# Performance work log

Measured on AMD Instinct MI355X. Metric: run time of the kernel, lower is better.

Reference implementation:

```python
import jax, jax.numpy as jnp
from jax import lax
import numpy as np

B = 128          # batch size
S = 207          # input spatial size implied by outputSpatialSize=[8,8]
N_PTS = 256000
NEG = -1e30      # -inf stand-in for masked max-pooling
# BNReLU channel counts in execution order: 8 resnet blocks x (bn1, bn2), final resnet BN(32), last BN(64)
SIZES = [8,8,8,8,8,16,16,16,16,24,24,24,24,32,32,32,32,64]
OFF = np.cumsum([0] + SIZES)

WSHAPES = dict(conv0=(3,3,1,8),
               c1a=(3,3,8,8), c1b=(3,3,8,8), c2a=(3,3,8,8), c2b=(3,3,8,8),
               c3a=(3,3,8,16), c3b=(3,3,16,16), c3r=(3,3,8,16),
               c4a=(3,3,16,16), c4b=(3,3,16,16),
               c5a=(3,3,16,24), c5b=(3,3,24,24), c5r=(3,3,16,24),
               c6a=(3,3,24,24), c6b=(3,3,24,24),
               c7a=(3,3,24,32), c7b=(3,3,32,32), c7r=(3,3,24,32),
               c8a=(3,3,32,32), c8b=(3,3,32,32),
               conv_last=(5,5,32,64))

def _conv(x, w, stride, padding):
    return lax.conv_general_dilated(x, w, (stride, stride), padding,
                                    dimension_numbers=('NHWC', 'HWIO', 'NHWC'))

def _pool_max(x, win, stride, init):
    return lax.reduce_window(x, init, lax.max, (1, win, win, 1), (1, stride, stride, 1), 'VALID')

def _bnrelu(x, m, g, b):
    # eval-mode BN folded to affine, applied on active sites only (inactive stay exactly 0)
    return m * jax.nn.relu(x * g + b)

def _subconv(x, w, m):
    # submanifold conv == dense conv on zero-filled grid, output restricted to active sites
    return _conv(x, w, 1, 'SAME') * m

def _strided(x, w, m, win, stride):
    # scn.Convolution: output site active iff any active input in its receptive field
    m2 = _pool_max(m, win, stride, 0.0)
    return _conv(x, w, stride, 'VALID') * m2, m2

def _block(x, m, g1, b1, w1, g2, b2, w2, wres, stride):
    # pre-activation basic block from scn.SparseResNet
    h = _bnrelu(x, m, g1, b1)
    if stride == 1:
        h, m2 = _subconv(h, w1, m), m
    else:
        h, m2 = _strided(h, w1, m, 3, 2)
    h = _subconv(_bnrelu(h, m2, g2, b2), w2, m2)
    r = x if wres is None else _strided(x, wres, m, 3, 2)[0]
    return h + r, m2

def _forward(locations, batch_idx, features, bn_gamma, bn_beta, W):
    idx = (batch_idx, locations[:, 0], locations[:, 1], jnp.zeros_like(batch_idx))
    x = jnp.zeros((B, S, S, 1), jnp.float32).at[idx].add(features[:, 0])  # InputLayer (sum dups)
    m = jnp.zeros((B, S, S, 1), jnp.float32).at[idx].set(1.0)             # active-site mask
    g = [bn_gamma[OFF[i]:OFF[i+1]] for i in range(len(SIZES))]
    b = [bn_beta[OFF[i]:OFF[i+1]] for i in range(len(SIZES))]
    x = _subconv(x, W['conv0'], m)                              # 1->8 @ 207x207
    # MaxPooling(pool 3, stride 2) over active sites only
    m2 = _pool_max(m, 3, 2, 0.0)
    x = jnp.where(m2 > 0, _pool_max(jnp.where(m > 0, x, NEG), 3, 2, NEG), 0.0)
    m = m2                                                      # @ 103x103
    blocks = [('c1a', 'c1b', None, 1), ('c2a', 'c2b', None, 1),
              ('c3a', 'c3b', 'c3r', 2), ('c4a', 'c4b', None, 1),
              ('c5a', 'c5b', 'c5r', 2), ('c6a', 'c6b', None, 1),
              ('c7a', 'c7b', 'c7r', 2), ('c8a', 'c8b', None, 1)]
    for i, (k1, k2, kr, st) in enumerate(blocks):
        x, m = _block(x, m, g[2*i], b[2*i], W[k1], g[2*i+1], b[2*i+1], W[k2],
                      None if kr is None else W[kr], st)        # 103->51->25->12
    x = _bnrelu(x, m, g[16], b[16])                             # final resnet BNReLU(32)
    x, m = _strided(x, W['conv_last'], m, 5, 1)                 # 32->64, 12x12 -> 8x8
    x = _bnrelu(x, m, g[17], b[17])
    flat = x.transpose(0, 3, 1, 2).reshape(B, -1)               # SparseToDense + flatten (NCHW order)
    return (flat @ W['w_lin'].T).reshape(B, -1, 1)              # [B, 100, 1]

def setup_inputs():
    key = jax.random.key(0)
    ks = iter(jax.random.split(key, 64))
    inp = {
        'locations': jax.random.randint(next(ks), (N_PTS, 2), 0, S, dtype=jnp.int32),
        'batch_idx': jax.random.randint(next(ks), (N_PTS,), 0, B, dtype=jnp.int32),
        'features': jax.random.normal(next(ks), (N_PTS, 1), jnp.float32),
        'bn_gamma': 1.0 + 0.1 * jax.random.normal(next(ks), (int(OFF[-1]),), jnp.float32),
        'bn_beta': 0.1 * jax.random.normal(next(ks), (int(OFF[-1]),), jnp.float32),
    }
    for name, shp in WSHAPES.items():
        fan_in = int(np.prod(shp[:-1]))
        inp[name] = jax.random.normal(next(ks), shp, jnp.float32) * (2.0 / fan_in) ** 0.5
    inp['w_lin'] = jax.random.normal(next(ks), (100, 64 * 8 * 8), jnp.float32) * (1.0 / 4096.0) ** 0.5
    return inp

def reference(locations, batch_idx, features, bn_gamma, bn_beta, conv0,
              c1a, c1b, c2a, c2b, c3a, c3b, c3r, c4a, c4b, c5a, c5b, c5r,
              c6a, c6b, c7a, c7b, c7r, c8a, c8b, conv_last, w_lin):
    W = dict(conv0=conv0, c1a=c1a, c1b=c1b, c2a=c2a, c2b=c2b, c3a=c3a, c3b=c3b, c3r=c3r,
             c4a=c4a, c4b=c4b, c5a=c5a, c5b=c5b, c5r=c5r, c6a=c6a, c6b=c6b,
             c7a=c7a, c7b=c7b, c7r=c7r, c8a=c8a, c8b=c8b, conv_last=conv_last, w_lin=w_lin)
    return _forward(locations, batch_idx, features, bn_gamma, bn_beta, W)
```

## Files before the change

kernel.cpp:

```cpp
#include <hip/hip_runtime.h>

#define S 207
#define BATCH 128
#define NPTS 256000

static const int OFFS[19] = {0,8,16,24,32,40,56,72,88,104,128,152,176,200,232,264,296,328,392};

__global__ void zero2_kernel(float4* __restrict__ a, float4* __restrict__ b, int n4) {
    int i = blockIdx.x * blockDim.x + threadIdx.x;
    if (i < n4) { a[i] = make_float4(0,0,0,0); b[i] = make_float4(0,0,0,0); }
}

__global__ void zero_kernel(float* __restrict__ p, int n) {
    int i = blockIdx.x * blockDim.x + threadIdx.x;
    if (i < n) p[i] = 0.0f;
}

__global__ void scatter_kernel(const int* __restrict__ loc, const int* __restrict__ bidx,
                               const float* __restrict__ feat,
                               float* __restrict__ xs, float* __restrict__ ms) {
    int t = blockIdx.x * blockDim.x + threadIdx.x;
    if (t >= NPTS) return;
    int b = bidx[t];
    int r = loc[2 * t];
    int c = loc[2 * t + 1];
    int idx = (b * S + r) * S + c;
    atomicAdd(&xs[idx], feat[t]);
    ms[idx] = 1.0f;
}

__global__ __launch_bounds__(256) void conv0_pool_kernel(
    const float* __restrict__ xs, const float* __restrict__ ms,
    const float* __restrict__ w,
    float* __restrict__ x1, float* __restrict__ m1) {
    const int Hout = 103;
    int opix = blockIdx.x * 256 + threadIdx.x;
    int total = BATCH * Hout * Hout;
    if (opix >= total) return;
    int wo = opix % Hout;
    int t = opix / Hout;
    int ho = t % Hout;
    int b  = t / Hout;

    float mv[3][3];
    float mwin = 0.0f;
    #pragma unroll
    for (int pi = 0; pi < 3; ++pi)
        #pragma unroll
        for (int pj = 0; pj < 3; ++pj) {
            float m = ms[(b * S + 2 * ho + pi) * S + 2 * wo + pj];
            mv[pi][pj] = m;
            mwin = fmaxf(mwin, m);
        }
    float* xp = x1 + (size_t)opix * 8;
    if (mwin <= 0.0f) {
        *(float4*)xp = make_float4(0,0,0,0);
        *(float4*)(xp + 4) = make_float4(0,0,0,0);
        m1[opix] = 0.0f;
        return;
    }
    float p[5][5];
    #pragma unroll
    for (int r = 0; r < 5; ++r) {
        int ii = 2 * ho - 1 + r;
        #pragma unroll
        for (int c = 0; c < 5; ++c) {
            int jj = 2 * wo - 1 + c;
            bool ok = ((unsigned)ii < (unsigned)S) && ((unsigned)jj < (unsigned)S);
            p[r][c] = ok ? xs[(b * S + ii) * S + jj] : 0.0f;
        }
    }
    float best[8];
    #pragma unroll
    for (int co = 0; co < 8; ++co) best[co] = -1e30f;
    #pragma unroll
    for (int pi = 0; pi < 3; ++pi)
        #pragma unroll
        for (int pj = 0; pj < 3; ++pj) {
            if (mv[pi][pj] > 0.0f) {
                float acc[8];
                #pragma unroll
                for (int co = 0; co < 8; ++co) acc[co] = 0.0f;
                #pragma unroll
                for (int kh = 0; kh < 3; ++kh)
                    #pragma unroll
                    for (int kw = 0; kw < 3; ++kw) {
                        float x = p[pi + kh][pj + kw];
                        #pragma unroll
                        for (int co = 0; co < 8; ++co)
                            acc[co] = fmaf(x, w[(kh * 3 + kw) * 8 + co], acc[co]);
                    }
                #pragma unroll
                for (int co = 0; co < 8; ++co) best[co] = fmaxf(best[co], acc[co]);
            }
        }
    *(float4*)xp = make_float4(best[0], best[1], best[2], best[3]);
    *(float4*)(xp + 4) = make_float4(best[4], best[5], best[6], best[7]);
    m1[opix] = 1.0f;
}

template <int C, int TILE, int NTX>
__global__ __launch_bounds__(256) void resblock_kernel(
    const float* __restrict__ in, const float* __restrict__ mask,
    const float* __restrict__ w1, const float* __restrict__ w2,
    const float* __restrict__ g1, const float* __restrict__ bb1,
    const float* __restrict__ g2, const float* __restrict__ bb2,
    float* __restrict__ out, int H) {
    constexpr int XT = TILE + 4, HT = TILE + 2;
    constexpr int XA = XT * XT, HA = HT * HT;
    __shared__ float xs[C][XA];
    __shared__ float h1[C][HA];
    __shared__ float msh[XA];

    int tid = threadIdx.x;
    int bid = blockIdx.x;
    int b = bid / (NTX * NTX);
    int t = bid % (NTX * NTX);
    int r0 = (t / NTX) * TILE, c0 = (t % NTX) * TILE;

    float gr[C], br[C];
    #pragma unroll
    for (int c = 0; c < C; ++c) { gr[c] = g1[c]; br[c] = bb1[c]; }

    for (int i = tid; i < XA; i += 256) {
        int py = i / XT, px = i % XT;
        int gy = r0 - 2 + py, gx = c0 - 2 + px;
        bool ok = (unsigned)gy < (unsigned)H && (unsigned)gx < (unsigned)H;
        float m = 0.0f;
        if (ok) m = mask[(size_t)(b * H + gy) * H + gx];
        msh[i] = m;
        if (m > 0.0f) {
            const float* ip = in + ((size_t)(b * H + gy) * H + gx) * C;
            #pragma unroll
            for (int c = 0; c < C; c += 4) {
                float4 x4 = *(const float4*)(ip + c);
                xs[c    ][i] = m * fmaxf(fmaf(x4.x, gr[c],     br[c]),     0.0f);
                xs[c + 1][i] = m * fmaxf(fmaf(x4.y, gr[c + 1], br[c + 1]), 0.0f);
                xs[c + 2][i] = m * fmaxf(fmaf(x4.z, gr[c + 2], br[c + 2]), 0.0f);
                xs[c + 3][i] = m * fmaxf(fmaf(x4.w, gr[c + 3], br[c + 3]), 0.0f);
            }
        } else {
            #pragma unroll
            for (int c = 0; c < C; ++c) xs[c][i] = 0.0f;
        }
    }
    #pragma unroll
    for (int c = 0; c < C; ++c) { gr[c] = g2[c]; br[c] = bb2[c]; }
    __syncthreads();

    for (int pos = tid; pos < HA; pos += 256) {
        int py = pos / HT, px = pos % HT;
        float mc = msh[(py + 1) * XT + px + 1];
        float acc[C];
        #pragma unroll
        for (int co = 0; co < C; ++co) acc[co] = 0.0f;
        if (mc > 0.0f) {
            #pragma unroll
            for (int kh = 0; kh < 3; ++kh)
                #pragma unroll
                for (int kw = 0; kw < 3; ++kw) {
                    int pix = (py + kh) * XT + px + kw;
                    const float* wp = w1 + (kh * 3 + kw) * C * C;
                    #pragma unroll
                    for (int ci = 0; ci < C; ++ci) {
                        float xv = xs[ci][pix];
                        #pragma unroll
                        for (int co = 0; co < C; ++co)
                            acc[co] = fmaf(xv, wp[ci * C + co], acc[co]);
                    }
                }
        }
        #pragma unroll
        for (int co = 0; co < C; ++co)
            h1[co][pos] = mc * fmaxf(fmaf(acc[co] * mc, gr[co], br[co]), 0.0f);
    }
    __syncthreads();

    for (int pos = tid; pos < TILE * TILE; pos += 256) {
        int ty = pos / TILE, tx = pos % TILE;
        int gy = r0 + ty, gx = c0 + tx;
        if (gy < H && gx < H) {
            float mo = msh[(ty + 2) * XT + tx + 2];
            float acc[C];
            #pragma unroll
            for (int co = 0; co < C; ++co) acc[co] = 0.0f;
            if (mo > 0.0f) {
                #pragma unroll
                for (int kh = 0; kh < 3; ++kh)
                    #pragma unroll
                    for (int kw = 0; kw < 3; ++kw) {
                        int pix = (ty + kh) * HT + tx + kw;
                        const float* wp = w2 + (kh * 3 + kw) * C * C;
                        #pragma unroll
                        for (int ci = 0; ci < C; ++ci) {
                            float xv = h1[ci][pix];
                            #pragma unroll
                            for (int co = 0; co < C; ++co)
                                acc[co] = fmaf(xv, wp[ci * C + co], acc[co]);
                        }
                    }
            }
            const float* rp = in + ((size_t)(b * H + gy) * H + gx) * C;
            float* op = out + ((size_t)(b * H + gy) * H + gx) * C;
            #pragma unroll
            for (int j = 0; j < C; j += 4) {
                float4 r4 = *(const float4*)(rp + j);
                float4 o4;
                o4.x = fmaf(acc[j],     mo, r4.x);
                o4.y = fmaf(acc[j + 1], mo, r4.y);
                o4.z = fmaf(acc[j + 2], mo, r4.z);
                o4.w = fmaf(acc[j + 3], mo, r4.w);
                *(float4*)(op + j) = o4;
            }
        }
    }
}

template <int K, int CIN, int COUT, int COT, bool BN, bool RES>
__global__ __launch_bounds__(256) void fconv_kernel(
    const float* __restrict__ in, const float* __restrict__ w,
    const float* __restrict__ g, const float* __restrict__ bbn,
    const float* __restrict__ mIn, const float* __restrict__ mOut,
    const float* __restrict__ res, float* __restrict__ out,
    int Hin, int Hout, int stride, int pad) {
    const int Win = Hin, Wout = Hout;
    int npix = BATCH * Hout * Wout;
    int opix = blockIdx.x * 256 + threadIdx.x;
    if (opix >= npix) return;
    int co0 = blockIdx.y * COT;
    int wo = opix % Wout;
    int t = opix / Wout;
    int ho = t % Hout;
    int b  = t / Hout;

    float mo = mOut[opix];
    float* op = out + (size_t)opix * COUT + co0;
    if (mo <= 0.0f) {
        #pragma unroll
        for (int j = 0; j < COT; j += 4) {
            float4 r4 = RES ? *(const float4*)(res + (size_t)opix * COUT + co0 + j)
                            : make_float4(0,0,0,0);
            *(float4*)(op + j) = r4;
        }
        return;
    }
    float acc[COT];
    #pragma unroll
    for (int j = 0; j < COT; ++j) acc[j] = 0.0f;

    #pragma unroll
    for (int kh = 0; kh < K; ++kh) {
        int ih = ho * stride + kh - pad;
        if ((unsigned)ih >= (unsigned)Hin) continue;
        #pragma unroll
        for (int kw = 0; kw < K; ++kw) {
            int iw = wo * stride + kw - pad;
            if ((unsigned)iw >= (unsigned)Win) continue;
            int ipix = (b * Hin + ih) * Win + iw;
            float mi = 1.0f;
            if (BN) { mi = mIn[ipix]; if (mi <= 0.0f) continue; }
            const float* ip = in + (size_t)ipix * CIN;
            const float* wp = w + (kh * K + kw) * CIN * COUT + co0;
            #pragma unroll
            for (int ci = 0; ci < CIN; ci += 4) {
                float4 xv = *(const float4*)(ip + ci);
                if (BN) {
                    xv.x = mi * fmaxf(fmaf(xv.x, g[ci],     bbn[ci]),     0.0f);
                    xv.y = mi * fmaxf(fmaf(xv.y, g[ci + 1], bbn[ci + 1]), 0.0f);
                    xv.z = mi * fmaxf(fmaf(xv.z, g[ci + 2], bbn[ci + 2]), 0.0f);
                    xv.w = mi * fmaxf(fmaf(xv.w, g[ci + 3], bbn[ci + 3]), 0.0f);
                }
                #pragma unroll
                for (int j = 0; j < COT; ++j) {
                    acc[j] = fmaf(xv.x, wp[(ci    ) * COUT + j], acc[j]);
                    acc[j] = fmaf(xv.y, wp[(ci + 1) * COUT + j], acc[j]);
                    acc[j] = fmaf(xv.z, wp[(ci + 2) * COUT + j], acc[j]);
                    acc[j] = fmaf(xv.w, wp[(ci + 3) * COUT + j], acc[j]);
                }
            }
        }
    }
    #pragma unroll
    for (int j = 0; j < COT; j += 4) {
        float4 o4;
        o4.x = acc[j] * mo; o4.y = acc[j+1] * mo; o4.z = acc[j+2] * mo; o4.w = acc[j+3] * mo;
        if (RES) {
            float4 r4 = *(const float4*)(res + (size_t)opix * COUT + co0 + j);
            o4.x += r4.x; o4.y += r4.y; o4.z += r4.z; o4.w += r4.w;
        }
        *(float4*)(op + j) = o4;
    }
}

template <int CIN, int COUT, int COT>
__global__ __launch_bounds__(256) void strided_both_kernel(
    const float* __restrict__ in,
    const float* __restrict__ wR, const float* __restrict__ wA,
    const float* __restrict__ g, const float* __restrict__ bbn,
    const float* __restrict__ mIn, float* __restrict__ mOutBuf,
    float* __restrict__ outR, float* __restrict__ outA,
    int Hin, int Hout) {
    int npix = BATCH * Hout * Hout;
    int opix = blockIdx.x * 256 + threadIdx.x;
    if (opix >= npix) return;
    int co0 = blockIdx.y * COT;
    int wo = opix % Hout;
    int t = opix / Hout;
    int ho = t % Hout;
    int b  = t / Hout;

    float accR[COT], accA[COT];
    #pragma unroll
    for (int j = 0; j < COT; ++j) { accR[j] = 0.0f; accA[j] = 0.0f; }
    float m2 = 0.0f;

    #pragma unroll
    for (int kh = 0; kh < 3; ++kh) {
        int ih = 2 * ho + kh;
        #pragma unroll
        for (int kw = 0; kw < 3; ++kw) {
            int iw = 2 * wo + kw;
            int ipix = (b * Hin + ih) * Hin + iw;
            float mi = mIn[ipix];
            if (mi <= 0.0f) continue;
            m2 = fmaxf(m2, mi);
            const float* ip  = in + (size_t)ipix * CIN;
            const float* wpR = wR + (kh * 3 + kw) * CIN * COUT + co0;
            const float* wpA = wA + (kh * 3 + kw) * CIN * COUT + co0;
            #pragma unroll
            for (int ci = 0; ci < CIN; ci += 4) {
                float4 xv = *(const float4*)(ip + ci);
                float4 xa;
                xa.x = mi * fmaxf(fmaf(xv.x, g[ci],     bbn[ci]),     0.0f);
                xa.y = mi * fmaxf(fmaf(xv.y, g[ci + 1], bbn[ci + 1]), 0.0f);
                xa.z = mi * fmaxf(fmaf(xv.z, g[ci + 2], bbn[ci + 2]), 0.0f);
                xa.w = mi * fmaxf(fmaf(xv.w, g[ci + 3], bbn[ci + 3]), 0.0f);
                #pragma unroll
                for (int j = 0; j < COT; ++j) {
                    accR[j] = fmaf(xv.x, wpR[(ci    ) * COUT + j], accR[j]);
                    accR[j] = fmaf(xv.y, wpR[(ci + 1) * COUT + j], accR[j]);
                    accR[j] = fmaf(xv.z, wpR[(ci + 2) * COUT + j], accR[j]);
                    accR[j] = fmaf(xv.w, wpR[(ci + 3) * COUT + j], accR[j]);
                    accA[j] = fmaf(xa.x, wpA[(ci    ) * COUT + j], accA[j]);
                    accA[j] = fmaf(xa.y, wpA[(ci + 1) * COUT + j], accA[j]);
                    accA[j] = fmaf(xa.z, wpA[(ci + 2) * COUT + j], accA[j]);
                    accA[j] = fmaf(xa.w, wpA[(ci + 3) * COUT + j], accA[j]);
                }
            }
        }
    }
    if (blockIdx.y == 0) mOutBuf[opix] = m2;
    float* opR = outR + (size_t)opix * COUT + co0;
    float* opA = outA + (size_t)opix * COUT + co0;
    #pragma unroll
    for (int j = 0; j < COT; j += 4) {
        *(float4*)(opR + j) = make_float4(accR[j] * m2, accR[j+1] * m2, accR[j+2] * m2, accR[j+3] * m2);
        *(float4*)(opA + j) = make_float4(accA[j] * m2, accA[j+1] * m2, accA[j+2] * m2, accA[j+3] * m2);
    }
}

__global__ __launch_bounds__(256) void convlast_kernel(
    const float* __restrict__ in,
    const float* __restrict__ w,
    const float* __restrict__ g, const float* __restrict__ bb,
    const float* __restrict__ mIn,
    float* __restrict__ part) {
    __shared__ float xs[32 * 97];
    __shared__ float ws[5 * 32 * 64];
    int b   = blockIdx.x;
    int kh  = blockIdx.y;
    int tid = threadIdx.x;
    for (int i = tid; i < 8 * 12 * 32; i += 256) {
        int ci = i & 31;
        int p  = i >> 5;
        int gpix = (b * 12 + kh + p / 12) * 12 + (p % 12);
        float m = mIn[gpix];
        float v = 0.0f;
        if (m > 0.0f) v = fmaxf(fmaf(in[(size_t)gpix * 32 + ci], g[ci], bb[ci]), 0.0f);
        xs[ci * 97 + p] = v;
    }
    {
        const float4* src = (const float4*)(w + kh * (5 * 32 * 64));
        float4* dst = (float4*)ws;
        for (int i = tid; i < 5 * 32 * 64 / 4; i += 256) dst[i] = src[i];
    }
    __syncthreads();

    int px = tid & 63;
    int cg = tid >> 6;
    int ho = px >> 3, wo = px & 7;
    float acc[16];
    #pragma unroll
    for (int j = 0; j < 16; ++j) acc[j] = 0.0f;
    #pragma unroll
    for (int kw = 0; kw < 5; ++kw) {
        const float* xp = xs + ho * 12 + wo + kw;
        const float* wp = ws + kw * (32 * 64) + cg * 16;
        #pragma unroll
        for (int ci = 0; ci < 32; ++ci) {
            float xv = xp[ci * 97];
            const float* wr = wp + ci * 64;
            #pragma unroll
            for (int j = 0; j < 16; j += 4) {
                float4 w4 = *(const float4*)(wr + j);
                acc[j]     = fmaf(xv, w4.x, acc[j]);
                acc[j + 1] = fmaf(xv, w4.y, acc[j + 1]);
                acc[j + 2] = fmaf(xv, w4.z, acc[j + 2]);
                acc[j + 3] = fmaf(xv, w4.w, acc[j + 3]);
            }
        }
    }
    float* op = part + ((((size_t)kh * BATCH + b) * 64 + px) * 64) + cg * 16;
    #pragma unroll
    for (int j = 0; j < 16; j += 4)
        *(float4*)(op + j) = make_float4(acc[j], acc[j+1], acc[j+2], acc[j+3]);
}

__global__ __launch_bounds__(256) void bn_tr_kernel(
    const float* __restrict__ part, const float* __restrict__ m,
    const float* __restrict__ g, const float* __restrict__ bb,
    float* __restrict__ xt) {
    int tid = blockIdx.x * 256 + threadIdx.x;
    if (tid >= BATCH * 4096) return;
    int c = tid & 63, hw = (tid >> 6) & 63, b = tid >> 12;
    float s = 0.0f;
    #pragma unroll
    for (int k = 0; k < 5; ++k)
        s += part[(((size_t)k * BATCH + b) * 64 + hw) * 64 + c];
    float v = m[b * 64 + hw] * fmaxf(fmaf(s, g[c], bb[c]), 0.0f);
    xt[((size_t)b << 12) + c * 64 + hw] = v;
}

__global__ void pool_kernel(const float* __restrict__ in, float* __restrict__ out,
                            int Hin, int Win, int Hout, int Wout, int win, int stride) {
    int tid = blockIdx.x * blockDim.x + threadIdx.x;
    int total = BATCH * Hout * Wout;
    if (tid >= total) return;
    int wo = tid % Wout;
    int p = tid / Wout;
    int ho = p % Hout;
    int b  = p / Hout;
    float mx = 0.0f;
    for (int i = 0; i < win; ++i)
        for (int j = 0; j < win; ++j)
            mx = fmaxf(mx, in[(b * Hin + ho * stride + i) * Win + wo * stride + j]);
    out[tid] = mx;
}

__global__ __launch_bounds__(256) void linear_gemm_kernel(
    const float* __restrict__ xt, const float* __restrict__ wl,
    float* __restrict__ out) {
    int o = blockIdx.x;
    int half = threadIdx.x >> 7;
    int b = threadIdx.x & 127;
    int k0 = blockIdx.y * 512 + half * 256;
    const float* xp = xt + ((size_t)b << 12) + k0;
    const float* wp = wl + o * 4096 + k0;
    float acc = 0.0f;
    #pragma unroll 16
    for (int k = 0; k < 256; k += 4) {
        float4 xv = *(const float4*)(xp + k);
        float4 wv = *(const float4*)(wp + k);
        acc = fmaf(xv.x, wv.x, acc); acc = fmaf(xv.y, wv.y, acc);
        acc = fmaf(xv.z, wv.z, acc); acc = fmaf(xv.w, wv.w, acc);
    }
    atomicAdd(&out[b * 100 + o], acc);
}

template <int K, int CIN, int COUT, int COT, bool BN, bool RES>
static inline void fconv(hipStream_t s, const float* in, const float* w,
                         const float* g, const float* bbn,
                         const float* mIn, const float* mOut, const float* res,
                         float* out, int Hin, int Hout, int stride, int pad) {
    int npix = BATCH * Hout * Hout;
    dim3 grid((npix + 255) / 256, COUT / COT);
    fconv_kernel<K, CIN, COUT, COT, BN, RES><<<grid, 256, 0, s>>>(
        in, w, g, bbn, mIn, mOut, res, out, Hin, Hout, stride, pad);
}

template <int CIN, int COUT, int COT>
static inline void strided_both(hipStream_t s, const float* in, const float* wR, const float* wA,
                                const float* g, const float* bbn, const float* mIn,
                                float* mOutBuf, float* outR, float* outA, int Hin, int Hout) {
    int npix = BATCH * Hout * Hout;
    dim3 grid((npix + 255) / 256, COUT / COT);
    strided_both_kernel<CIN, COUT, COT><<<grid, 256, 0, s>>>(
        in, wR, wA, g, bbn, mIn, mOutBuf, outR, outA, Hin, Hout);
}

extern "C" void kernel_launch(void* const* d_in, const int* in_sizes, int n_in,
                              void* d_out, int out_size, void* d_ws, size_t ws_size,
                              hipStream_t stream) {
    const int*   loc   = (const int*)d_in[0];
    const int*   bidx  = (const int*)d_in[1];
    const float* feat  = (const float*)d_in[2];
    const float* gamma = (const float*)d_in[3];
    const float* beta  = (const float*)d_in[4];
    const float* Wconv0 = (const float*)d_in[5];
    const float* Wc1a = (const float*)d_in[6];
    const float* Wc1b = (const float*)d_in[7];
    const float* Wc2a = (const float*)d_in[8];
    const float* Wc2b = (const float*)d_in[9];
    const float* Wc3a = (const float*)d_in[10];
    const float* Wc3b = (const float*)d_in[11];
    const float* Wc3r = (const float*)d_in[12];
    const float* Wc4a = (const float*)d_in[13];
    const float* Wc4b = (const float*)d_in[14];
    const float* Wc5a = (const float*)d_in[15];
    const float* Wc5b = (const float*)d_in[16];
    const float* Wc5r = (const float*)d_in[17];
    const float* Wc6a = (const float*)d_in[18];
    const float* Wc6b = (const float*)d_in[19];
    const float* Wc7a = (const float*)d_in[20];
    const float* Wc7b = (const float*)d_in[21];
    const float* Wc7r = (const float*)d_in[22];
    const float* Wc8a = (const float*)d_in[23];
    const float* Wc8b = (const float*)d_in[24];
    const float* Wlast = (const float*)d_in[25];
    const float* wlin  = (const float*)d_in[26];

    const size_t SZB = (size_t)BATCH * 103 * 103 * 8;
    const size_t SZM = (size_t)BATCH * 103 * 103;
    float* b0 = (float*)d_ws;
    float* b1 = b0 + SZB;
    float* b2 = b1 + SZB;
    float* m0 = b2 + SZB;
    float* m1 = m0 + SZM;

    const float* G[18];
    const float* Bt[18];
    for (int i = 0; i < 18; ++i) { G[i] = gamma + OFFS[i]; Bt[i] = beta + OFFS[i]; }

    {
        int n = BATCH * S * S;
        zero2_kernel<<<(n / 4 + 255) / 256, 256, 0, stream>>>((float4*)b1, (float4*)b2, n / 4);
        scatter_kernel<<<(NPTS + 255) / 256, 256, 0, stream>>>(loc, bidx, feat, b1, b2);
        int total = BATCH * 103 * 103;
        conv0_pool_kernel<<<(total + 255) / 256, 256, 0, stream>>>(b1, b2, Wconv0, b0, m0);
    }

    resblock_kernel<8, 16, 7><<<dim3(7 * 7 * BATCH), 256, 0, stream>>>(
        b0, m0, Wc1a, Wc1b, G[0], Bt[0], G[1], Bt[1], b1, 103);
    resblock_kernel<8, 16, 7><<<dim3(7 * 7 * BATCH), 256, 0, stream>>>(
        b1, m0, Wc2a, Wc2b, G[2], Bt[2], G[3], Bt[3], b2, 103);
    strided_both<8, 16, 16>(stream, b2, Wc3r, Wc3a, G[4], Bt[4], m0, m1, b0, b1, 103, 51);
    fconv<3, 16, 16, 8, true, true >(stream, b1, Wc3b, G[5], Bt[5], m1, m1, b0, b2, 51, 51, 1, 1);
    fconv<3, 16, 16, 8, true, false>(stream, b2, Wc4a, G[6], Bt[6], m1, m1, nullptr, b0, 51, 51, 1, 1);
    fconv<3, 16, 16, 8, true, true >(stream, b0, Wc4b, G[7], Bt[7], m1, m1, b2,      b1, 51, 51, 1, 1);
    strided_both<16, 24, 12>(stream, b1, Wc5r, Wc5a, G[8], Bt[8], m1, m0, b0, b2, 51, 25);
    fconv<3, 24, 24, 8, true, true >(stream, b2, Wc5b, G[9], Bt[9], m0, m0, b0, b1, 25, 25, 1, 1);
    fconv<3, 24, 24, 8, true, false>(stream, b1, Wc6a, G[10], Bt[10], m0, m0, nullptr, b0, 25, 25, 1, 1);
    fconv<3, 24, 24, 8, true, true >(stream, b0, Wc6b, G[11], Bt[11], m0, m0, b1,      b2, 25, 25, 1, 1);
    strided_both<24, 32, 8>(stream, b2, Wc7r, Wc7a, G[12], Bt[12], m0, m1, b0, b1, 25, 12);
    fconv<3, 32, 32, 4, true, true >(stream, b1, Wc7b, G[13], Bt[13], m1, m1, b0, b2, 12, 12, 1, 1);
    fconv<3, 32, 32, 4, true, false>(stream, b2, Wc8a, G[14], Bt[14], m1, m1, nullptr, b0, 12, 12, 1, 1);
    fconv<3, 32, 32, 4, true, true >(stream, b0, Wc8b, G[15], Bt[15], m1, m1, b2,      b1, 12, 12, 1, 1);
    pool_kernel<<<(BATCH * 64 + 255) / 256, 256, 0, stream>>>(m1, m0, 12, 12, 8, 8, 5, 1);
    convlast_kernel<<<dim3(BATCH, 5), 256, 0, stream>>>(b1, Wlast, G[16], Bt[16], m1, b0);
    bn_tr_kernel<<<(BATCH * 4096 + 255) / 256, 256, 0, stream>>>(b0, m0, G[17], Bt[17], b2);
    zero_kernel<<<(BATCH * 100 + 255) / 256, 256, 0, stream>>>((float*)d_out, BATCH * 100);
    linear_gemm_kernel<<<dim3(100, 8), 256, 0, stream>>>(b2, wlin, (float*)d_out);
}
```

Baseline: 741.4 us.

## Compact active sites into shared lists in the fused 8-channel resblock

```diff
diff --git a/kernel.cpp b/kernel.cpp
--- a/kernel.cpp
+++ b/kernel.cpp
@@ -99,18 +99,21 @@
     m1[opix] = 1.0f;
 }
 
-template <int C, int TILE, int NTX>
-__global__ __launch_bounds__(256) void resblock_kernel(
+__global__ __launch_bounds__(256) void resblock8_kernel(
     const float* __restrict__ in, const float* __restrict__ mask,
     const float* __restrict__ w1, const float* __restrict__ w2,
     const float* __restrict__ g1, const float* __restrict__ bb1,
     const float* __restrict__ g2, const float* __restrict__ bb2,
     float* __restrict__ out, int H) {
+    constexpr int TILE = 16, NTX = 7;
     constexpr int XT = TILE + 4, HT = TILE + 2;
     constexpr int XA = XT * XT, HA = HT * HT;
-    __shared__ float xs[C][XA];
-    __shared__ float h1[C][HA];
+    constexpr int T2 = TILE * TILE;
+    __shared__ float4 xsa[XA], xsb[XA];
+    __shared__ float4 h1a[HA], h1b[HA];
     __shared__ float msh[XA];
+    __shared__ unsigned short list2[HA], list3[T2];
+    __shared__ int cnt2, cnt3;
 
     int tid = threadIdx.x;
     int bid = blockIdx.x;
@@ -118,9 +121,11 @@
     int t = bid % (NTX * NTX);
     int r0 = (t / NTX) * TILE, c0 = (t % NTX) * TILE;
 
-    float gr[C], br[C];
-    #pragma unroll
-    for (int c = 0; c < C; ++c) { gr[c] = g1[c]; br[c] = bb1[c]; }
+    if (tid == 0) { cnt2 = 0; cnt3 = 0; }
+
+    float g1r[8], b1r[8];
+    #pragma unroll
+    for (int c = 0; c < 8; ++c) { g1r[c] = g1[c]; b1r[c] = bb1[c]; }
 
     for (int i = tid; i < XA; i += 256) {
         int py = i / XT, px = i % XT;
@@ -129,90 +134,127 @@
         float m = 0.0f;
         if (ok) m = mask[(size_t)(b * H + gy) * H + gx];
         msh[i] = m;
+        float4 va = make_float4(0,0,0,0), vb = make_float4(0,0,0,0);
         if (m > 0.0f) {
-            const float* ip = in + ((size_t)(b * H + gy) * H + gx) * C;
+            const float* ip = in + ((size_t)(b * H + gy) * H + gx) * 8;
+            float4 x0 = *(const float4*)ip;
+            float4 x1 = *(const float4*)(ip + 4);
+            va.x = fmaxf(fmaf(x0.x, g1r[0], b1r[0]), 0.0f);
+            va.y = fmaxf(fmaf(x0.y, g1r[1], b1r[1]), 0.0f);
+            va.z = fmaxf(fmaf(x0.z, g1r[2], b1r[2]), 0.0f);
+            va.w = fmaxf(fmaf(x0.w, g1r[3], b1r[3]), 0.0f);
+            vb.x = fmaxf(fmaf(x1.x, g1r[4], b1r[4]), 0.0f);
+            vb.y = fmaxf(fmaf(x1.y, g1r[5], b1r[5]), 0.0f);
+            vb.z = fmaxf(fmaf(x1.z, g1r[6], b1r[6]), 0.0f);
+            vb.w = fmaxf(fmaf(x1.w, g1r[7], b1r[7]), 0.0f);
+        }
+        xsa[i] = va; xsb[i] = vb;
+    }
+    float g2r[8], b2r[8];
+    #pragma unroll
+    for (int c = 0; c < 8; ++c) { g2r[c] = g2[c]; b2r[c] = bb2[c]; }
+    __syncthreads();
+
+    for (int i = tid; i < HA; i += 256) {
+        h1a[i] = make_float4(0,0,0,0);
+        h1b[i] = make_float4(0,0,0,0);
+        int py = i / HT, px = i % HT;
+        if (msh[(py + 1) * XT + px + 1] > 0.0f) {
+            int k = atomicAdd(&cnt2, 1);
+            list2[k] = (unsigned short)i;
+        }
+    }
+    for (int i = tid; i < T2; i += 256) {
+        int ty = i / TILE, tx = i % TILE;
+        if (r0 + ty < H && c0 + tx < H && msh[(ty + 2) * XT + tx + 2] > 0.0f) {
+            int k = atomicAdd(&cnt3, 1);
+            list3[k] = (unsigned short)i;
+        }
+    }
+    __syncthreads();
+
+    int n2 = cnt2;
+    for (int k = tid; k < n2; k += 256) {
+        int pos = list2[k];
+        int py = pos / HT, px = pos % HT;
+        float acc[8];
+        #pragma unroll
+        for (int co = 0; co < 8; ++co) acc[co] = 0.0f;
+        #pragma unroll
+        for (int kh = 0; kh < 3; ++kh)
             #pragma unroll
-            for (int c = 0; c < C; c += 4) {
-                float4 x4 = *(const float4*)(ip + c);
-                xs[c    ][i] = m * fmaxf(fmaf(x4.x, gr[c],     br[c]),     0.0f);
-                xs[c + 1][i] = m * fmaxf(fmaf(x4.y, gr[c + 1], br[c + 1]), 0.0f);
-                xs[c + 2][i] = m * fmaxf(fmaf(x4.z, gr[c + 2], br[c + 2]), 0.0f);
-                xs[c + 3][i] = m * fmaxf(fmaf(x4.w, gr[c + 3], br[c + 3]), 0.0f);
+            for (int kw = 0; kw < 3; ++kw) {
+                int pix = (py + kh) * XT + px + kw;
+                float4 a = xsa[pix], c4 = xsb[pix];
+                const float* wp = w1 + (kh * 3 + kw) * 64;
+                #pragma unroll
+                for (int co = 0; co < 8; ++co) {
+                    float s = fmaf(a.x,  wp[co],      acc[co]);
+                    s = fmaf(a.y,  wp[8  + co], s);
+                    s = fmaf(a.z,  wp[16 + co], s);
+                    s = fmaf(a.w,  wp[24 + co], s);
+                    s = fmaf(c4.x, wp[32 + co], s);
+                    s = fmaf(c4.y, wp[40 + co], s);
+                    s = fmaf(c4.z, wp[48 + co], s);
+                    acc[co] = fmaf(c4.w, wp[56 + co], s);
+                }
             }
-        } else {
-            #pragma unroll
-            for (int c = 0; c < C; ++c) xs[c][i] = 0.0f;
-        }
-    }
-    #pragma unroll
-    for (int c = 0; c < C; ++c) { gr[c] = g2[c]; br[c] = bb2[c]; }
+        float4 ha, hb;
+        ha.x = fmaxf(fmaf(acc[0], g2r[0], b2r[0]), 0.0f);
+        ha.y = fmaxf(fmaf(acc[1], g2r[1], b2r[1]), 0.0f);
+        ha.z = fmaxf(fmaf(acc[2], g2r[2], b2r[2]), 0.0f);
+        ha.w = fmaxf(fmaf(acc[3], g2r[3], b2r[3]), 0.0f);
+        hb.x = fmaxf(fmaf(acc[4], g2r[4], b2r[4]), 0.0f);
+        hb.y = fmaxf(fmaf(acc[5], g2r[5], b2r[5]), 0.0f);
+        hb.z = fmaxf(fmaf(acc[6], g2r[6], b2r[6]), 0.0f);
+        hb.w = fmaxf(fmaf(acc[7], g2r[7], b2r[7]), 0.0f);
+        h1a[pos] = ha; h1b[pos] = hb;
+    }
     __syncthreads();
 
-    for (int pos = tid; pos < HA; pos += 256) {
-        int py = pos / HT, px = pos % HT;
-        float mc = msh[(py + 1) * XT + px + 1];
-        float acc[C];
-        #pragma unroll
-        for (int co = 0; co < C; ++co) acc[co] = 0.0f;
-        if (mc > 0.0f) {
-            #pragma unroll
-            for (int kh = 0; kh < 3; ++kh)
-                #pragma unroll
-                for (int kw = 0; kw < 3; ++kw) {
-                    int pix = (py + kh) * XT + px + kw;
-                    const float* wp = w1 + (kh * 3 + kw) * C * C;
-                    #pragma unroll
-                    for (int ci = 0; ci < C; ++ci) {
-                        float xv = xs[ci][pix];
-                        #pragma unroll
-                        for (int co = 0; co < C; ++co)
-                            acc[co] = fmaf(xv, wp[ci * C + co], acc[co]);
-                    }
-                }
-        }
-        #pragma unroll
-        for (int co = 0; co < C; ++co)
-            h1[co][pos] = mc * fmaxf(fmaf(acc[co] * mc, gr[co], br[co]), 0.0f);
-    }
-    __syncthreads();
-
-    for (int pos = tid; pos < TILE * TILE; pos += 256) {
+    for (int i = tid; i < T2; i += 256) {
+        int ty = i / TILE, tx = i % TILE;
+        int gy = r0 + ty, gx = c0 + tx;
+        if (gy < H && gx < H && msh[(ty + 2) * XT + tx + 2] <= 0.0f) {
+            const float* rp = in + ((size_t)(b * H + gy) * H + gx) * 8;
+            float* op = out + ((size_t)(b * H + gy) * H + gx) * 8;
+            *(float4*)op = *(const float4*)rp;
+            *(float4*)(op + 4) = *(const float4*)(rp + 4);
+        }
+    }
+    int n3 = cnt3;
+    for (int k = tid; k < n3; k += 256) {
+        int pos = list3[k];
         int ty = pos / TILE, tx = pos % TILE;
         int gy = r0 + ty, gx = c0 + tx;
-        if (gy < H && gx < H) {
-            float mo = msh[(ty + 2) * XT + tx + 2];
-            float acc[C];
+        float acc[8];
+        #pragma unroll
+        for (int co = 0; co < 8; ++co) acc[co] = 0.0f;
+        #pragma unroll
+        for (int kh = 0; kh < 3; ++kh)
             #pragma unroll
-            for (int co = 0; co < C; ++co) acc[co] = 0.0f;
-            if (mo > 0.0f) {
+            for (int kw = 0; kw < 3; ++kw) {
+                int pix = (ty + kh) * HT + tx + kw;
+                float4 a = h1a[pix], c4 = h1b[pix];
+                const float* wp = w2 + (kh * 3 + kw) * 64;
                 #pragma unroll
-                for (int kh = 0; kh < 3; ++kh)
-                    #pragma unroll
-                    for (int kw = 0; kw < 3; ++kw) {
-                        int pix = (ty + kh) * HT + tx + kw;
-                        const float* wp = w2 + (kh * 3 + kw) * C * C;
-                        #pragma unroll
-                        for (int ci = 0; ci < C; ++ci) {
-                            float xv = h1[ci][pix];
-                            #pragma unroll
-                            for (int co = 0; co < C; ++co)
-                                acc[co] = fmaf(xv, wp[ci * C + co], acc[co]);
-                        }
-                    }
+                for (int co = 0; co < 8; ++co) {
+                    float s = fmaf(a.x,  wp[co],      acc[co]);
+                    s = fmaf(a.y,  wp[8  + co], s);
+                    s = fmaf(a.z,  wp[16 + co], s);
+                    s = fmaf(a.w,  wp[24 + co], s);
+                    s = fmaf(c4.x, wp[32 + co], s);
+                    s = fmaf(c4.y, wp[40 + co], s);
+                    s = fmaf(c4.z, wp[48 + co], s);
+                    acc[co] = fmaf(c4.w, wp[56 + co], s);
+                }
             }
-            const float* rp = in + ((size_t)(b * H + gy) * H + gx) * C;
-            float* op = out + ((size_t)(b * H + gy) * H + gx) * C;
-            #pragma unroll
-            for (int j = 0; j < C; j += 4) {
-                float4 r4 = *(const float4*)(rp + j);
-                float4 o4;
-                o4.x = fmaf(acc[j],     mo, r4.x);
-                o4.y = fmaf(acc[j + 1], mo, r4.y);
-                o4.z = fmaf(acc[j + 2], mo, r4.z);
-                o4.w = fmaf(acc[j + 3], mo, r4.w);
-                *(float4*)(op + j) = o4;
-            }
-        }
+        const float* rp = in + ((size_t)(b * H + gy) * H + gx) * 8;
+        float* op = out + ((size_t)(b * H + gy) * H + gx) * 8;
+        float4 ra = *(const float4*)rp;
+        float4 rb = *(const float4*)(rp + 4);
+        *(float4*)op       = make_float4(acc[0] + ra.x, acc[1] + ra.y, acc[2] + ra.z, acc[3] + ra.w);
+        *(float4*)(op + 4) = make_float4(acc[4] + rb.x, acc[5] + rb.y, acc[6] + rb.z, acc[7] + rb.w);
     }
 }
 
@@ -539,9 +581,9 @@
         conv0_pool_kernel<<<(total + 255) / 256, 256, 0, stream>>>(b1, b2, Wconv0, b0, m0);
     }
 
-    resblock_kernel<8, 16, 7><<<dim3(7 * 7 * BATCH), 256, 0, stream>>>(
+    resblock8_kernel<<<dim3(7 * 7 * BATCH), 256, 0, stream>>>(
         b0, m0, Wc1a, Wc1b, G[0], Bt[0], G[1], Bt[1], b1, 103);
-    resblock_kernel<8, 16, 7><<<dim3(7 * 7 * BATCH), 256, 0, stream>>>(
+    resblock8_kernel<<<dim3(7 * 7 * BATCH), 256, 0, stream>>>(
         b1, m0, Wc2a, Wc2b, G[2], Bt[2], G[3], Bt[3], b2, 103);
     strided_both<8, 16, 16>(stream, b2, Wc3r, Wc3a, G[4], Bt[4], m0, m1, b0, b1, 103, 51);
     fconv<3, 16, 16, 8, true, true >(stream, b1, Wc3b, G[5], Bt[5], m1, m1, b0, b2, 51, 51, 1, 1);
```

After: 899.6 us. 21.3% more time.

## Add LDS-tiled 16-channel submanifold conv kernel for stage-3 layers

Applied to the files above, without the earlier changes.

```diff
diff --git a/kernel.cpp b/kernel.cpp
--- a/kernel.cpp
+++ b/kernel.cpp
@@ -213,6 +213,127 @@
                 *(float4*)(op + j) = o4;
             }
         }
+    }
+}
+
+template <bool RES>
+__global__ __launch_bounds__(256) void fconv16_lds_kernel(
+    const float* __restrict__ in, const float* __restrict__ w,
+    const float* __restrict__ g, const float* __restrict__ bbn,
+    const float* __restrict__ mask, const float* __restrict__ res,
+    float* __restrict__ out, int H, int NTX) {
+    constexpr int TILE = 16, XT = TILE + 2;
+    constexpr int XA = XT * XT;
+    __shared__ float4 xs[4][XA];
+    __shared__ float  wsh[9 * 16 * 16];
+    __shared__ float  msh[XA];
+
+    int tid = threadIdx.x;
+    int bid = blockIdx.x;
+    int b = bid / (NTX * NTX);
+    int t = bid % (NTX * NTX);
+    int r0 = (t / NTX) * TILE, c0 = (t % NTX) * TILE;
+
+    {
+        const float4* src = (const float4*)w;
+        float4* dst = (float4*)wsh;
+        for (int i = tid; i < 9 * 16 * 16 / 4; i += 256) dst[i] = src[i];
+    }
+    for (int i = tid; i < XA; i += 256) {
+        int py = i / XT, px = i % XT;
+        int gy = r0 - 1 + py, gx = c0 - 1 + px;
+        bool ok = (unsigned)gy < (unsigned)H && (unsigned)gx < (unsigned)H;
+        float m = ok ? mask[(size_t)(b * H + gy) * H + gx] : 0.0f;
+        msh[i] = m;
+        float4 v0 = make_float4(0,0,0,0), v1 = v0, v2 = v0, v3 = v0;
+        if (m > 0.0f) {
+            const float* ip = in + ((size_t)(b * H + gy) * H + gx) * 16;
+            float4 x0 = *(const float4*)(ip);
+            float4 x1 = *(const float4*)(ip + 4);
+            float4 x2 = *(const float4*)(ip + 8);
+            float4 x3 = *(const float4*)(ip + 12);
+            v0.x = fmaxf(fmaf(x0.x, g[0],  bbn[0]),  0.0f);
+            v0.y = fmaxf(fmaf(x0.y, g[1],  bbn[1]),  0.0f);
+            v0.z = fmaxf(fmaf(x0.z, g[2],  bbn[2]),  0.0f);
+            v0.w = fmaxf(fmaf(x0.w, g[3],  bbn[3]),  0.0f);
+            v1.x = fmaxf(fmaf(x1.x, g[4],  bbn[4]),  0.0f);
+            v1.y = fmaxf(fmaf(x1.y, g[5],  bbn[5]),  0.0f);
+            v1.z = fmaxf(fmaf(x1.z, g[6],  bbn[6]),  0.0f);
+            v1.w = fmaxf(fmaf(x1.w, g[7],  bbn[7]),  0.0f);
+            v2.x = fmaxf(fmaf(x2.x, g[8],  bbn[8]),  0.0f);
+            v2.y = fmaxf(fmaf(x2.y, g[9],  bbn[9]),  0.0f);
+            v2.z = fmaxf(fmaf(x2.z, g[10], bbn[10]), 0.0f);
+            v2.w = fmaxf(fmaf(x2.w, g[11], bbn[11]), 0.0f);
+            v3.x = fmaxf(fmaf(x3.x, g[12], bbn[12]), 0.0f);
+            v3.y = fmaxf(fmaf(x3.y, g[13], bbn[13]), 0.0f);
+            v3.z = fmaxf(fmaf(x3.z, g[14], bbn[14]), 0.0f);
+            v3.w = fmaxf(fmaf(x3.w, g[15], bbn[15]), 0.0f);
+        }
+        xs[0][i] = v0; xs[1][i] = v1; xs[2][i] = v2; xs[3][i] = v3;
+    }
+    __syncthreads();
+
+    int ty = tid >> 4, tx = tid & 15;
+    int gy = r0 + ty, gx = c0 + tx;
+    if (gy >= H || gx >= H) return;
+    size_t opix = (size_t)(b * H + gy) * H + gx;
+    float mo = msh[(ty + 1) * XT + tx + 1];
+    float* op = out + opix * 16;
+    if (mo <= 0.0f) {
+        #pragma unroll
+        for (int j = 0; j < 16; j += 4) {
+            float4 r4 = RES ? *(const float4*)(res + opix * 16 + j) : make_float4(0,0,0,0);
+            *(float4*)(op + j) = r4;
+        }
+        return;
+    }
+    float acc[16];
+    #pragma unroll
+    for (int j = 0; j < 16; ++j) acc[j] = 0.0f;
+    #pragma unroll
+    for (int kh = 0; kh < 3; ++kh)
+        #pragma unroll
+        for (int kw = 0; kw < 3; ++kw) {
+            int pix = (ty + kh) * XT + tx + kw;
+            const float* wp = wsh + (kh * 3 + kw) * 256;
+            #pragma unroll
+            for (int q = 0; q < 4; ++q) {
+                float4 xv = xs[q][pix];
+                const float* wr = wp + q * 64;
+                #pragma unroll
+                for (int j = 0; j < 16; j += 4) {
+                    float4 wa = *(const float4*)(wr + j);
+                    float4 wb = *(const float4*)(wr + 16 + j);
+                    float4 wc = *(const float4*)(wr + 32 + j);
+                    float4 wd = *(const float4*)(wr + 48 + j);
+                    acc[j]     = fmaf(xv.x, wa.x, acc[j]);
+                    acc[j + 1] = fmaf(xv.x, wa.y, acc[j + 1]);
+                    acc[j + 2] = fmaf(xv.x, wa.z, acc[j + 2]);
+                    acc[j + 3] = fmaf(xv.x, wa.w, acc[j + 3]);
+                    acc[j]     = fmaf(xv.y, wb.x, acc[j]);
+                    acc[j + 1] = fmaf(xv.y, wb.y, acc[j + 1]);
+                    acc[j + 2] = fmaf(xv.y, wb.z, acc[j + 2]);
+                    acc[j + 3] = fmaf(xv.y, wb.w, acc[j + 3]);
+                    acc[j]     = fmaf(xv.z, wc.x, acc[j]);
+                    acc[j + 1] = fmaf(xv.z, wc.y, acc[j + 1]);
+                    acc[j + 2] = fmaf(xv.z, wc.z, acc[j + 2]);
+                    acc[j + 3] = fmaf(xv.z, wc.w, acc[j + 3]);
+                    acc[j]     = fmaf(xv.w, wd.x, acc[j]);
+                    acc[j + 1] = fmaf(xv.w, wd.y, acc[j + 1]);
+                    acc[j + 2] = fmaf(xv.w, wd.z, acc[j + 2]);
+                    acc[j + 3] = fmaf(xv.w, wd.w, acc[j + 3]);
+                }
+            }
+        }
+    #pragma unroll
+    for (int j = 0; j < 16; j += 4) {
+        float4 o4;
+        o4.x = acc[j] * mo; o4.y = acc[j+1] * mo; o4.z = acc[j+2] * mo; o4.w = acc[j+3] * mo;
+        if (RES) {
+            float4 r4 = *(const float4*)(res + opix * 16 + j);
+            o4.x += r4.x; o4.y += r4.y; o4.z += r4.z; o4.w += r4.w;
+        }
+        *(float4*)(op + j) = o4;
     }
 }
 
@@ -544,9 +665,12 @@
     resblock_kernel<8, 16, 7><<<dim3(7 * 7 * BATCH), 256, 0, stream>>>(
         b1, m0, Wc2a, Wc2b, G[2], Bt[2], G[3], Bt[3], b2, 103);
     strided_both<8, 16, 16>(stream, b2, Wc3r, Wc3a, G[4], Bt[4], m0, m1, b0, b1, 103, 51);
-    fconv<3, 16, 16, 8, true, true >(stream, b1, Wc3b, G[5], Bt[5], m1, m1, b0, b2, 51, 51, 1, 1);
-    fconv<3, 16, 16, 8, true, false>(stream, b2, Wc4a, G[6], Bt[6], m1, m1, nullptr, b0, 51, 51, 1, 1);
-    fconv<3, 16, 16, 8, true, true >(stream, b0, Wc4b, G[7], Bt[7], m1, m1, b2,      b1, 51, 51, 1, 1);
+    fconv16_lds_kernel<true><<<dim3(16 * BATCH), 256, 0, stream>>>(
+        b1, Wc3b, G[5], Bt[5], m1, b0, b2, 51, 4);
+    fconv16_lds_kernel<false><<<dim3(16 * BATCH), 256, 0, stream>>>(
+        b2, Wc4a, G[6], Bt[6], m1, nullptr, b0, 51, 4);
+    fconv16_lds_kernel<true><<<dim3(16 * BATCH), 256, 0, stream>>>(
+        b0, Wc4b, G[7], Bt[7], m1, b2, b1, 51, 4);
     strided_both<16, 24, 12>(stream, b1, Wc5r, Wc5a, G[8], Bt[8], m1, m0, b0, b2, 51, 25);
     fconv<3, 24, 24, 8, true, true >(stream, b2, Wc5b, G[9], Bt[9], m0, m0, b0, b1, 25, 25, 1, 1);
     fconv<3, 24, 24, 8, true, false>(stream, b1, Wc6a, G[10], Bt[10], m0, m0, nullptr, b0, 25, 25, 1, 1);
```

New measurement: 761.1 us. 2.7% more time.
